# Kernel optimization log

Hardware: AMD Instinct MI355X
Metric: run time of the kernel (lower is better)

The kernel has to match this reference:

```python
import jax, jax.numpy as jnp
import numpy as np

V, E, HS, HD = 32000, 64, 128, 128
S, T = 128, 48


def gru_cell(x, h, Wih, Whh, bih, bhh):
    # torch nn.GRU cell: gates stacked as [r, z, n]
    gi = x @ Wih.T + bih
    gh = h @ Whh.T + bhh
    ir, iz, inn = jnp.split(gi, 3, axis=-1)
    hr, hz, hn = jnp.split(gh, 3, axis=-1)
    r = jax.nn.sigmoid(ir + hr)
    z = jax.nn.sigmoid(iz + hz)
    n = jnp.tanh(inn + r * hn)
    return (1.0 - z) * n + z * h


def setup_inputs() -> dict:
    key = jax.random.key(0)
    ks = jax.random.split(key, 16)
    sc = 0.05
    inp = {
        'document': jax.random.randint(ks[0], (S, T), 0, V, dtype=jnp.int64),
        'enc_emb': jax.random.normal(ks[1], (V, E), jnp.float32) * sc,
        'enc_Wih': jax.random.normal(ks[2], (3 * HS, E), jnp.float32) * sc,
        'enc_Whh': jax.random.normal(ks[3], (3 * HS, HS), jnp.float32) * sc,
        'enc_bih': jax.random.normal(ks[4], (3 * HS,), jnp.float32) * sc,
        'enc_bhh': jax.random.normal(ks[5], (3 * HS,), jnp.float32) * sc,
        'doc_Wih': jax.random.normal(ks[6], (3 * HD, HS), jnp.float32) * sc,
        'doc_Whh': jax.random.normal(ks[7], (3 * HD, HD), jnp.float32) * sc,
        'doc_bih': jax.random.normal(ks[8], (3 * HD,), jnp.float32) * sc,
        'doc_bhh': jax.random.normal(ks[9], (3 * HD,), jnp.float32) * sc,
        'dec_emb': jax.random.normal(ks[10], (V, E), jnp.float32) * sc,
        'dec_Wih': jax.random.normal(ks[11], (3 * HS, E + HD), jnp.float32) * sc,
        'dec_Whh': jax.random.normal(ks[12], (3 * HS, HS), jnp.float32) * sc,
        'dec_bih': jax.random.normal(ks[13], (3 * HS,), jnp.float32) * sc,
        'dec_bhh': jax.random.normal(ks[14], (3 * HS,), jnp.float32) * sc,
        'fc_W': jax.random.normal(ks[15], (V, HS), jnp.float32) * sc,
        'fc_b': jnp.zeros((V,), jnp.float32),
    }
    return inp


def reference(document, enc_emb, enc_Wih, enc_Whh, enc_bih, enc_bhh,
              doc_Wih, doc_Whh, doc_bih, doc_bhh,
              dec_emb, dec_Wih, dec_Whh, dec_bih, dec_bhh, fc_W, fc_b):
    s, t = document.shape
    # --- sentence encoder: GRU over tokens, batch = sentences ---
    x = enc_emb[document]                       # [S, T, E]
    def enc_step(h, xt):
        return gru_cell(xt, h, enc_Wih, enc_Whh, enc_bih, enc_bhh), None
    h0 = jnp.zeros((s, HS), enc_emb.dtype)
    sent_vec, _ = jax.lax.scan(enc_step, h0, jnp.swapaxes(x, 0, 1))  # [S, HS]
    # --- document encoder: GRU over sentence vectors, batch = 1 ---
    def doc_step(h, sv):
        return gru_cell(sv[None, :], h, doc_Wih, doc_Whh, doc_bih, doc_bhh), None
    hd0 = jnp.zeros((1, HD), enc_emb.dtype)
    doc_h, _ = jax.lax.scan(doc_step, hd0, sent_vec)
    doc_vec = doc_h[0]                          # [HD]
    # --- teacher-forced decoder, vectorized over sentences ---
    dec_in = dec_emb[document[:, :-1]]          # [S, T-1, E]
    ctx = jnp.broadcast_to(doc_vec, (s, t - 1, HD))
    xs = jnp.swapaxes(jnp.concatenate([dec_in, ctx], axis=-1), 0, 1)  # [T-1, S, E+HD]
    def dec_step(h, xt):
        h2 = gru_cell(xt, h, dec_Wih, dec_Whh, dec_bih, dec_bhh)
        logits = h2 @ fc_W.T + fc_b
        return h2, logits
    _, logits = jax.lax.scan(dec_step, sent_vec, xs)  # [T-1, S, V]
    targets = document[:, 1:].T                 # [T-1, S]
    logp = jax.nn.log_softmax(logits, axis=-1)
    ll = jnp.take_along_axis(logp, targets[..., None], axis=-1)[..., 0]
    # per-sentence mean over steps, then mean over sentences == global mean
    return -jnp.mean(ll)
```

## Files before the change

kernel.cpp:

```cpp
#include <hip/hip_runtime.h>

typedef unsigned short ushort_t;
typedef short bf16x8 __attribute__((ext_vector_type(8)));
typedef float f32x4 __attribute__((ext_vector_type(4)));
typedef unsigned int u32x4 __attribute__((ext_vector_type(4)));
typedef _Float16 half2t __attribute__((ext_vector_type(2)));

#define LOG2E 1.4426950408889634f
#define LN2   0.6931471805599453f

__device__ __forceinline__ float bf2f(ushort_t u) {
    union { unsigned int i; float f; } v; v.i = ((unsigned int)u) << 16; return v.f;
}
__device__ __forceinline__ ushort_t f2bf(float f) {
    union { float f; unsigned int i; } v; v.f = f;
    unsigned int u = v.i;
    unsigned int r = (u + 0x7FFFu + ((u >> 16) & 1u)) >> 16;
    return (ushort_t)r;
}
__device__ __forceinline__ float hsum4(f32x4 v) { return (v[0] + v[1]) + (v[2] + v[3]); }
__device__ __forceinline__ float frcp(float x) { return __builtin_amdgcn_rcpf(x); }
__device__ __forceinline__ float fsig(float x) { return frcp(1.f + __expf(-x)); }
__device__ __forceinline__ float ftanh(float x) { return 1.f - 2.f * frcp(1.f + __expf(2.f * x)); }
__device__ __forceinline__ int hpad(int e) { return e + ((e >> 4) << 2); }
__device__ __forceinline__ float dot2(unsigned int w, unsigned int h, float acc) {
    union { unsigned int u; half2t h2; } a, b;
    a.u = w; b.u = h;
    return __builtin_amdgcn_fdot2(a.h2, b.h2, acc, false);
}
__device__ __forceinline__ float dpp_xor1_add(float x) {
    int m = __builtin_amdgcn_update_dpp(0, __builtin_bit_cast(int, x), 0xB1, 0xF, 0xF, true);
    return x + __builtin_bit_cast(float, m);
}
__device__ __forceinline__ float dpp_xor2_add(float x) {
    int m = __builtin_amdgcn_update_dpp(0, __builtin_bit_cast(int, x), 0x4E, 0xF, 0xF, true);
    return x + __builtin_bit_cast(float, m);
}
__device__ __forceinline__ ushort_t f2h(float f) {
    union { _Float16 h; ushort_t s; } c; c.h = (_Float16)f; return c.s;
}

__global__ void k_convert(const float* __restrict__ w, ushort_t* __restrict__ o,
                          const float* __restrict__ fcb, float* __restrict__ fcbs) {
    int i = blockIdx.x * blockDim.x + threadIdx.x;
    if (i < 1024000) {
        f32x4 v = ((const f32x4*)w)[i];
        union { ushort_t u[4]; unsigned long long q; } p;
        p.u[0] = f2bf(v[0] * LOG2E); p.u[1] = f2bf(v[1] * LOG2E);
        p.u[2] = f2bf(v[2] * LOG2E); p.u[3] = f2bf(v[3] * LOG2E);
        ((unsigned long long*)o)[i] = p.q;
    } else if (i < 1024000 + 8000) {
        int k = i - 1024000;
        f32x4 b = ((const f32x4*)fcb)[k];
        ((f32x4*)fcbs)[k] = b * LOG2E;
    }
}

__global__ __launch_bounds__(768, 1) void k_encoder(
    const int* __restrict__ doc, const float* __restrict__ emb,
    const float* __restrict__ Wih, const float* __restrict__ Whh,
    const float* __restrict__ bih, const float* __restrict__ bhh,
    float* __restrict__ sent) {
    int s = blockIdx.x, t = threadIdx.x;
    int half = t & 1, j = t >> 1;
    __shared__ float xs[80], hs[160];
    __shared__ float gi[384], gh[384];
    __shared__ int toks[48];
    f32x4 wih[8], whh[16];
#pragma unroll
    for (int k = 0; k < 8; k++) wih[k] = *(const f32x4*)(Wih + j * 64 + half * 32 + k * 4);
#pragma unroll
    for (int k = 0; k < 16; k++) whh[k] = *(const f32x4*)(Whh + j * 128 + half * 64 + k * 4);
    float bi = bih[j], bh = bhh[j];
    if (t < 48) toks[t] = doc[s * 48 + t];
    if (t < 128) hs[hpad(t)] = 0.f;
    __syncthreads();
    if (t < 64) xs[hpad(t)] = emb[(size_t)toks[0] * 64 + t];
    __syncthreads();
    const float* xb = xs + half * 40;
    const float* hb = hs + half * 80;
    for (int tt = 0; tt < 48; tt++) {
        float xnext = (t < 64 && tt + 1 < 48) ? emb[(size_t)toks[tt + 1] * 64 + t] : 0.f;
        f32x4 a0 = {0,0,0,0}, b0 = {0,0,0,0}, b1 = {0,0,0,0};
#pragma unroll
        for (int k = 0; k < 8; k++) a0 += wih[k] * (*(const f32x4*)(xb + k * 4 + (k >> 2) * 4));
#pragma unroll
        for (int k = 0; k < 16; k += 2) {
            b0 += whh[k] * (*(const f32x4*)(hb + k * 4 + (k >> 2) * 4));
            b1 += whh[k + 1] * (*(const f32x4*)(hb + (k + 1) * 4 + ((k + 1) >> 2) * 4));
        }
        float a = hsum4(a0), b = hsum4(b0 + b1);
        a = dpp_xor1_add(a); b = dpp_xor1_add(b);
        if (half == 0) { gi[j] = a + bi; gh[j] = b + bh; }
        __syncthreads();
        if (t < 128) {
            float r = fsig(gi[t] + gh[t]);
            float z = fsig(gi[t + 128] + gh[t + 128]);
            float n = ftanh(gi[t + 256] + r * gh[t + 256]);
            hs[hpad(t)] = (1.f - z) * n + z * hs[hpad(t)];
        }
        if (t < 64 && tt + 1 < 48) xs[hpad(t)] = xnext;
        __syncthreads();
    }
    if (t < 128) sent[s * 128 + t] = hs[hpad(t)];
}

__global__ void k_doc_gi(const float* __restrict__ sv, const float* __restrict__ Wih,
                         const float* __restrict__ bih, float* __restrict__ gidoc,
                         const float* __restrict__ Whh, ushort_t* __restrict__ wdoc) {
    int bid = blockIdx.x, j = threadIdx.x;
    if (bid >= 128) {
        int i = (bid - 128) * 384 + j;
        if (i < 12288) {
            f32x4 v = ((const f32x4*)Whh)[i];
            union { ushort_t u[4]; unsigned long long q; } p;
            p.u[0] = f2h(v[0]); p.u[1] = f2h(v[1]); p.u[2] = f2h(v[2]); p.u[3] = f2h(v[3]);
            ((unsigned long long*)wdoc)[i] = p.q;
        }
        return;
    }
    __shared__ f32x4 v4[32];
    if (j < 128) ((float*)v4)[j] = sv[bid * 128 + j];
    __syncthreads();
    f32x4 a0 = {0,0,0,0}, a1 = {0,0,0,0};
#pragma unroll
    for (int k = 0; k < 32; k += 2) {
        a0 += *(const f32x4*)(Wih + j * 128 + k * 4) * v4[k];
        a1 += *(const f32x4*)(Wih + j * 128 + (k + 1) * 4) * v4[k + 1];
    }
    gidoc[bid * 384 + j] = bih[j] + hsum4(a0 + a1);
}

__global__ __launch_bounds__(512, 1) __attribute__((amdgpu_waves_per_eu(1, 2)))
void k_doc_seq(
    const float* __restrict__ gidoc, const ushort_t* __restrict__ wdoc,
    const float* __restrict__ bhh, float* __restrict__ dvec) {
    int t = threadIdx.x, q = t & 3, e = t >> 2;
    __shared__ unsigned int hpk[2][64];
    u32x4 wr4[4], wz4[4], wn4[4];
    const ushort_t* wbase = wdoc + e * 128 + q * 32;
#pragma unroll
    for (int k = 0; k < 4; k++) {
        wr4[k] = *(const u32x4*)(wbase + k * 8);
        wz4[k] = *(const u32x4*)(wbase + 128 * 128 + k * 8);
        wn4[k] = *(const u32x4*)(wbase + 256 * 128 + k * 8);
    }
    float biasr = bhh[e], biasz = bhh[128 + e], biasn = bhh[256 + e];
    float cr = gidoc[e], cz = gidoc[128 + e], cn = gidoc[256 + e];
    if (t < 64) hpk[0][t] = 0u;
    float he = 0.f;
    __syncthreads();
    for (int i = 0; i < 128; i++) {
        float nr = 0.f, nz = 0.f, nn = 0.f;
        if (i + 1 < 128) {
            const float* g = gidoc + (i + 1) * 384;
            nr = g[e]; nz = g[128 + e]; nn = g[256 + e];
        }
        const unsigned int* hp = &hpk[i & 1][q * 16];
        u32x4 hv[4];
        hv[0] = *(const u32x4*)(hp);
        hv[1] = *(const u32x4*)(hp + 4);
        hv[2] = *(const u32x4*)(hp + 8);
        hv[3] = *(const u32x4*)(hp + 12);
        float ra0 = 0.f, ra1 = 0.f, za0 = 0.f, za1 = 0.f, na0 = 0.f, na1 = 0.f;
#pragma unroll
        for (int k = 0; k < 4; k++) {
            u32x4 h4 = hv[k];
            ra0 = dot2(wr4[k][0], h4[0], ra0); ra1 = dot2(wr4[k][1], h4[1], ra1);
            ra0 = dot2(wr4[k][2], h4[2], ra0); ra1 = dot2(wr4[k][3], h4[3], ra1);
            za0 = dot2(wz4[k][0], h4[0], za0); za1 = dot2(wz4[k][1], h4[1], za1);
            za0 = dot2(wz4[k][2], h4[2], za0); za1 = dot2(wz4[k][3], h4[3], za1);
            na0 = dot2(wn4[k][0], h4[0], na0); na1 = dot2(wn4[k][1], h4[1], na1);
            na0 = dot2(wn4[k][2], h4[2], na0); na1 = dot2(wn4[k][3], h4[3], na1);
        }
        float rp = ra0 + ra1, zp = za0 + za1, np = na0 + na1;
        rp = dpp_xor2_add(dpp_xor1_add(rp));
        zp = dpp_xor2_add(dpp_xor1_add(zp));
        np = dpp_xor2_add(dpp_xor1_add(np));
        float r = fsig(cr + rp + biasr);
        float z = fsig(cz + zp + biasz);
        float n = ftanh(cn + r * (np + biasn));
        he = (1.f - z) * n + z * he;
        if (q == 0) ((ushort_t*)&hpk[(i & 1) ^ 1][0])[e] = f2h(he);
        __syncthreads();
        cr = nr; cz = nz; cn = nn;
    }
    if (q == 0) dvec[e] = he;
}

__global__ __launch_bounds__(768, 1) void k_dec_gi(
    const int* __restrict__ doc, const float* __restrict__ emb,
    const float* __restrict__ Wih, const float* __restrict__ bih,
    const float* __restrict__ dvec, float* __restrict__ gidec) {
    int s = blockIdx.x, t = threadIdx.x, half = t & 1, j = t >> 1;
    __shared__ float xs[80], dvs[160];
    __shared__ int toks[48];
    f32x4 wih[8];
#pragma unroll
    for (int k = 0; k < 8; k++) wih[k] = *(const f32x4*)(Wih + j * 192 + half * 32 + k * 4);
    if (t < 128) dvs[hpad(t)] = dvec[t];
    if (t < 47) toks[t] = doc[s * 48 + t];
    __syncthreads();
    f32x4 c0 = {0,0,0,0}, c1 = {0,0,0,0};
    const float* dp = dvs + half * 80;
#pragma unroll
    for (int k = 0; k < 16; k += 2) {
        c0 += (*(const f32x4*)(Wih + j * 192 + 64 + half * 64 + k * 4)) *
              (*(const f32x4*)(dp + k * 4 + (k >> 2) * 4));
        c1 += (*(const f32x4*)(Wih + j * 192 + 64 + half * 64 + (k + 1) * 4)) *
              (*(const f32x4*)(dp + (k + 1) * 4 + ((k + 1) >> 2) * 4));
    }
    float g = hsum4(c0 + c1);
    g = dpp_xor1_add(g);
    g += bih[j];
    if (t < 64) xs[hpad(t)] = emb[(size_t)toks[0] * 64 + t];
    __syncthreads();
    const float* xb = xs + half * 40;
    for (int tt = 0; tt < 47; tt++) {
        float xnext = (t < 64 && tt + 1 < 47) ? emb[(size_t)toks[tt + 1] * 64 + t] : 0.f;
        f32x4 a0 = {0,0,0,0};
#pragma unroll
        for (int k = 0; k < 8; k++) a0 += wih[k] * (*(const f32x4*)(xb + k * 4 + (k >> 2) * 4));
        float a = hsum4(a0);
        a = dpp_xor1_add(a);
        if (half == 0) gidec[(tt * 128 + s) * 384 + j] = g + a;
        __syncthreads();
        if (t < 64 && tt + 1 < 47) xs[hpad(t)] = xnext;
        __syncthreads();
    }
}

__global__ __launch_bounds__(768, 1) void k_dec_seq(
    const float* __restrict__ gidec, const float* __restrict__ Whh,
    const float* __restrict__ bhh, const float* __restrict__ sent,
    ushort_t* __restrict__ h2b) {
    int s = blockIdx.x, t = threadIdx.x, half = t & 1, j = t >> 1;
    __shared__ float hs[160];
    __shared__ float gi[384], gh[384];
    f32x4 whh[16];
#pragma unroll
    for (int k = 0; k < 16; k++) whh[k] = *(const f32x4*)(Whh + j * 128 + half * 64 + k * 4);
    float bh = bhh[j];
    if (t < 128) hs[hpad(t)] = sent[s * 128 + t];
    float gval = (half == 0) ? gidec[s * 384 + j] : 0.f;
    __syncthreads();
    const float* hb = hs + half * 80;
    for (int i = 0; i < 47; i++) {
        float gnext = (half == 0 && i + 1 < 47) ? gidec[((i + 1) * 128 + s) * 384 + j] : 0.f;
        f32x4 b0 = {0,0,0,0}, b1 = {0,0,0,0};
#pragma unroll
        for (int k = 0; k < 16; k += 2) {
            b0 += whh[k] * (*(const f32x4*)(hb + k * 4 + (k >> 2) * 4));
            b1 += whh[k + 1] * (*(const f32x4*)(hb + (k + 1) * 4 + ((k + 1) >> 2) * 4));
        }
        float b = hsum4(b0 + b1);
        b = dpp_xor1_add(b);
        if (half == 0) { gh[j] = b + bh; gi[j] = gval; }
        __syncthreads();
        if (t < 128) {
            float r = fsig(gi[t] + gh[t]);
            float z = fsig(gi[t + 128] + gh[t + 128]);
            float n = ftanh(gi[t + 256] + r * gh[t + 256]);
            float hn = (1.f - z) * n + z * hs[hpad(t)];
            hs[hpad(t)] = hn;
            h2b[(i * 128 + s) * 128 + t] = f2bf(hn);
        }
        __syncthreads();
        gval = gnext;
    }
}

__global__ void k_tl(const int* __restrict__ doc, const ushort_t* __restrict__ h2b,
                     const ushort_t* __restrict__ wb, const float* __restrict__ fcb,
                     float* __restrict__ tl) {
    int r = blockIdx.x * 4 + (threadIdx.x >> 6);
    int lane = threadIdx.x & 63;
    int s = r & 127, t = r >> 7;
    int tok = doc[s * 48 + t + 1];
    const ushort_t* hp = h2b + r * 128;
    const ushort_t* wp = wb + tok * 128;
    float acc = bf2f(hp[lane]) * bf2f(wp[lane]) + bf2f(hp[lane + 64]) * bf2f(wp[lane + 64]);
#pragma unroll
    for (int m = 32; m >= 1; m >>= 1) acc += __shfl_xor(acc, m);
    if (lane == 0) tl[r] = acc * LN2 + fcb[tok];
}

#define LSE_VC 10
#define LSE_NC 3200
#define LSE_NPAIR 25
__global__ __launch_bounds__(512, 2) void k_lse(
    const ushort_t* __restrict__ h2b, const ushort_t* __restrict__ wb,
    const float* __restrict__ fcbs, float* __restrict__ parts) {
    int rb = blockIdx.x / LSE_VC;
    int vc = blockIdx.x % LSE_VC;
    int t = threadIdx.x;
    int wave = t >> 6, lane = t & 63;
    int rg = wave >> 1, cg = wave & 1;
    int q = lane >> 4, l15 = lane & 15;

    __shared__ __align__(16) char ldsB[65536];

    int row0 = rb * 128 + rg * 32;
    bf16x8 a[2][4];
    const ushort_t* ap = h2b + (size_t)(row0 + l15) * 128 + q * 8;
#pragma unroll
    for (int m = 0; m < 2; m++)
#pragma unroll
        for (int c = 0; c < 4; c++) a[m][c] = *(const bf16x8*)(ap + m * 2048 + c * 32);

    const char* wbB = (const char*)wb;
    int so = ((t >> 4) << 8) + (((t & 15) ^ ((t >> 4) & 15)) << 4);
    char* dst1 = ldsB + wave * 1024;

#define LSE_STAGE(buf, cb) do { \
    const char* g_ = wbB + (size_t)(cb) * 256 + so; \
    char* d_ = dst1 + (buf) * 16384; \
    __builtin_amdgcn_global_load_lds((const __attribute__((address_space(1))) unsigned int*)(g_), \
                                     (__attribute__((address_space(3))) unsigned int*)(d_), 16, 0, 0); \
    __builtin_amdgcn_global_load_lds((const __attribute__((address_space(1))) unsigned int*)(g_ + 8192), \
                                     (__attribute__((address_space(3))) unsigned int*)(d_ + 8192), 16, 0, 0); \
} while (0)

    int ra[2][4];
#pragma unroll
    for (int c2 = 0; c2 < 2; c2++)
#pragma unroll
        for (int c = 0; c < 4; c++)
            ra[c2][c] = (cg * 32 + c2 * 16 + l15) * 256 + (((q + 4 * c) ^ l15) << 4);

    int cb0 = vc * LSE_NC;
    f32x4 se[2] = {{0,0,0,0},{0,0,0,0}};

    LSE_STAGE(0, cb0);
    LSE_STAGE(1, cb0 + 64);
    __syncthreads();
    int cur = 0;
    for (int it = 0; it < LSE_NPAIR; ++it) {
        if (it + 1 < LSE_NPAIR) {
            LSE_STAGE(2 * (cur ^ 1),     cb0 + (2 * it + 2) * 64);
            LSE_STAGE(2 * (cur ^ 1) + 1, cb0 + (2 * it + 3) * 64);
        }
        int colg = cb0 + 2 * it * 64 + cg * 32 + l15;
        float bA0 = fcbs[colg],      bA1 = fcbs[colg + 16];
        float bB0 = fcbs[colg + 64], bB1 = fcbs[colg + 80];
#pragma unroll
        for (int half = 0; half < 2; half++) {
            const char* bb = ldsB + (size_t)(2 * cur + half) * 16384;
            float bs0 = half ? bB0 : bA0;
            float bs1 = half ? bB1 : bA1;
            f32x4 acc[2][2] = {{{0,0,0,0},{0,0,0,0}},{{0,0,0,0},{0,0,0,0}}};
#pragma unroll
            for (int c = 0; c < 4; c++) {
                bf16x8 b0 = *(const bf16x8*)(bb + ra[0][c]);
                bf16x8 b1 = *(const bf16x8*)(bb + ra[1][c]);
                acc[0][0] = __builtin_amdgcn_mfma_f32_16x16x32_bf16(a[0][c], b0, acc[0][0], 0, 0, 0);
                acc[1][0] = __builtin_amdgcn_mfma_f32_16x16x32_bf16(a[1][c], b0, acc[1][0], 0, 0, 0);
                acc[0][1] = __builtin_amdgcn_mfma_f32_16x16x32_bf16(a[0][c], b1, acc[0][1], 0, 0, 0);
                acc[1][1] = __builtin_amdgcn_mfma_f32_16x16x32_bf16(a[1][c], b1, acc[1][1], 0, 0, 0);
            }
#pragma unroll
            for (int m = 0; m < 2; m++) {
#pragma unroll
                for (int r = 0; r < 4; r++)
                    se[m][r] += __builtin_amdgcn_exp2f(acc[m][0][r] + bs0)
                              + __builtin_amdgcn_exp2f(acc[m][1][r] + bs1);
            }
        }
        __syncthreads();
        cur ^= 1;
    }

#pragma unroll
    for (int m = 0; m < 2; m++) {
        f32x4 v = se[m];
#pragma unroll
        for (int d = 1; d < 16; d <<= 1) {
            v[0] += __shfl_xor(v[0], d);
            v[1] += __shfl_xor(v[1], d);
            v[2] += __shfl_xor(v[2], d);
            v[3] += __shfl_xor(v[3], d);
        }
        if (l15 == 0) {
            float* p = parts + (size_t)(vc * 2 + cg) * 6016 + row0 + m * 16 + q * 4;
            p[0] = v[0]; p[1] = v[1]; p[2] = v[2]; p[3] = v[3];
        }
    }
}

__global__ void k_final1(const float* __restrict__ parts, const float* __restrict__ tl,
                         float* __restrict__ rowloss) {
    int r = blockIdx.x * 128 + threadIdx.x;
    float tot = 0.f;
#pragma unroll 4
    for (int c = 0; c < 20; c++) tot += parts[(size_t)c * 6016 + r];
    rowloss[r] = logf(tot) - tl[r];
}

__global__ void k_final2(const float* __restrict__ rowloss, float* __restrict__ out) {
    __shared__ float red[512];
    int tid = threadIdx.x;
    float acc = 0.f;
    for (int r = tid; r < 6016; r += 512) acc += rowloss[r];
    red[tid] = acc;
    __syncthreads();
    for (int s = 256; s > 0; s >>= 1) {
        if (tid < s) red[tid] += red[tid + s];
        __syncthreads();
    }
    if (tid == 0) out[0] = red[0] / 6016.f;
}

extern "C" void kernel_launch(void* const* d_in, const int* in_sizes, int n_in,
                              void* d_out, int out_size, void* d_ws, size_t ws_size,
                              hipStream_t stream) {
    const int* doc = (const int*)d_in[0];
    const float* enc_emb = (const float*)d_in[1];
    const float* enc_Wih = (const float*)d_in[2];
    const float* enc_Whh = (const float*)d_in[3];
    const float* enc_bih = (const float*)d_in[4];
    const float* enc_bhh = (const float*)d_in[5];
    const float* doc_Wih = (const float*)d_in[6];
    const float* doc_Whh = (const float*)d_in[7];
    const float* doc_bih = (const float*)d_in[8];
    const float* doc_bhh = (const float*)d_in[9];
    const float* dec_emb = (const float*)d_in[10];
    const float* dec_Wih = (const float*)d_in[11];
    const float* dec_Whh = (const float*)d_in[12];
    const float* dec_bih = (const float*)d_in[13];
    const float* dec_bhh = (const float*)d_in[14];
    const float* fc_W = (const float*)d_in[15];
    const float* fc_b = (const float*)d_in[16];

    char* ws = (char*)d_ws;
    ushort_t* fcWb = (ushort_t*)(ws + 0);
    float* sent    = (float*)(ws + 8192000);
    float* dvec    = (float*)(ws + 8257536);
    float* gidoc   = (float*)(ws + 8258048);
    float* gidec   = (float*)(ws + 8456192);
    ushort_t* h2b  = (ushort_t*)(ws + 17696768);
    float* tl      = (float*)(ws + 19236864);
    float* parts   = (float*)(ws + 19260928);
    float* rowloss = (float*)(ws + 20223488);
    ushort_t* wdoc = (ushort_t*)(ws + 20247552);
    float* fcbs    = (float*)(ws + 20345856);
    float* out = (float*)d_out;

    k_convert<<<4032, 256, 0, stream>>>(fc_W, fcWb, fc_b, fcbs);
    k_encoder<<<128, 768, 0, stream>>>(doc, enc_emb, enc_Wih, enc_Whh, enc_bih, enc_bhh, sent);
    k_doc_gi<<<160, 384, 0, stream>>>(sent, doc_Wih, doc_bih, gidoc, doc_Whh, wdoc);
    k_doc_seq<<<1, 512, 0, stream>>>(gidoc, wdoc, doc_bhh, dvec);
    k_dec_gi<<<128, 768, 0, stream>>>(doc, dec_emb, dec_Wih, dec_bih, dvec, gidec);
    k_dec_seq<<<128, 768, 0, stream>>>(gidec, dec_Whh, dec_bhh, sent, h2b);
    k_tl<<<1504, 256, 0, stream>>>(doc, h2b, fcWb, fc_b, tl);
    k_lse<<<47 * LSE_VC, 512, 0, stream>>>(h2b, fcWb, fcbs, parts);
    k_final1<<<47, 128, 0, stream>>>(parts, tl, rowloss);
    k_final2<<<1, 512, 0, stream>>>(rowloss, out);
}
```

Measured before the change: 267.5 us.

## Merge doc GRU, decoder input projection and fc_W conversion into one launch

Combines the serial single-block document GRU, the decoder embedding-input projection and the fc_W bf16 conversion into one kernel with role-split blocks. The independent stages can then run concurrently instead of one after another behind the long serial doc recurrence. To make the decoder input projection independent of the document vector, the context term (dec_Wih context columns times doc_vec, plus bias) moves to a tiny new kernel and is added in the decoder sequence kernel. The cost is one extra small launch and a mixed-role kernel whose block scheduling order decides how much overlap is actually achieved.

```diff
diff --git a/kernel.cpp b/kernel.cpp
--- a/kernel.cpp
+++ b/kernel.cpp
@@ -38,22 +38,6 @@
 }
 __device__ __forceinline__ ushort_t f2h(float f) {
     union { _Float16 h; ushort_t s; } c; c.h = (_Float16)f; return c.s;
-}
-
-__global__ void k_convert(const float* __restrict__ w, ushort_t* __restrict__ o,
-                          const float* __restrict__ fcb, float* __restrict__ fcbs) {
-    int i = blockIdx.x * blockDim.x + threadIdx.x;
-    if (i < 1024000) {
-        f32x4 v = ((const f32x4*)w)[i];
-        union { ushort_t u[4]; unsigned long long q; } p;
-        p.u[0] = f2bf(v[0] * LOG2E); p.u[1] = f2bf(v[1] * LOG2E);
-        p.u[2] = f2bf(v[2] * LOG2E); p.u[3] = f2bf(v[3] * LOG2E);
-        ((unsigned long long*)o)[i] = p.q;
-    } else if (i < 1024000 + 8000) {
-        int k = i - 1024000;
-        f32x4 b = ((const f32x4*)fcb)[k];
-        ((f32x4*)fcbs)[k] = b * LOG2E;
-    }
 }
 
 __global__ __launch_bounds__(768, 1) void k_encoder(
@@ -132,108 +116,134 @@
 }
 
 __global__ __launch_bounds__(512, 1) __attribute__((amdgpu_waves_per_eu(1, 2)))
-void k_doc_seq(
+void k_mid(
     const float* __restrict__ gidoc, const ushort_t* __restrict__ wdoc,
-    const float* __restrict__ bhh, float* __restrict__ dvec) {
-    int t = threadIdx.x, q = t & 3, e = t >> 2;
-    __shared__ unsigned int hpk[2][64];
-    u32x4 wr4[4], wz4[4], wn4[4];
-    const ushort_t* wbase = wdoc + e * 128 + q * 32;
-#pragma unroll
-    for (int k = 0; k < 4; k++) {
-        wr4[k] = *(const u32x4*)(wbase + k * 8);
-        wz4[k] = *(const u32x4*)(wbase + 128 * 128 + k * 8);
-        wn4[k] = *(const u32x4*)(wbase + 256 * 128 + k * 8);
-    }
-    float biasr = bhh[e], biasz = bhh[128 + e], biasn = bhh[256 + e];
-    float cr = gidoc[e], cz = gidoc[128 + e], cn = gidoc[256 + e];
-    if (t < 64) hpk[0][t] = 0u;
-    float he = 0.f;
-    __syncthreads();
-    for (int i = 0; i < 128; i++) {
-        float nr = 0.f, nz = 0.f, nn = 0.f;
-        if (i + 1 < 128) {
-            const float* g = gidoc + (i + 1) * 384;
-            nr = g[e]; nz = g[128 + e]; nn = g[256 + e];
-        }
-        const unsigned int* hp = &hpk[i & 1][q * 16];
-        u32x4 hv[4];
-        hv[0] = *(const u32x4*)(hp);
-        hv[1] = *(const u32x4*)(hp + 4);
-        hv[2] = *(const u32x4*)(hp + 8);
-        hv[3] = *(const u32x4*)(hp + 12);
-        float ra0 = 0.f, ra1 = 0.f, za0 = 0.f, za1 = 0.f, na0 = 0.f, na1 = 0.f;
+    const float* __restrict__ dbhh, float* __restrict__ dvec,
+    const int* __restrict__ doc, const float* __restrict__ demb,
+    const float* __restrict__ dWih, float* __restrict__ gidec,
+    const float* __restrict__ fcW, ushort_t* __restrict__ fcWb,
+    const float* __restrict__ fcb, float* __restrict__ fcbs) {
+    int bid = blockIdx.x, t = threadIdx.x;
+
+    if (bid == 0) {
+        int q = t & 3, e = t >> 2;
+        __shared__ unsigned int hpk[2][64];
+        u32x4 wr4[4], wz4[4], wn4[4];
+        const ushort_t* wbase = wdoc + e * 128 + q * 32;
 #pragma unroll
         for (int k = 0; k < 4; k++) {
-            u32x4 h4 = hv[k];
-            ra0 = dot2(wr4[k][0], h4[0], ra0); ra1 = dot2(wr4[k][1], h4[1], ra1);
-            ra0 = dot2(wr4[k][2], h4[2], ra0); ra1 = dot2(wr4[k][3], h4[3], ra1);
-            za0 = dot2(wz4[k][0], h4[0], za0); za1 = dot2(wz4[k][1], h4[1], za1);
-            za0 = dot2(wz4[k][2], h4[2], za0); za1 = dot2(wz4[k][3], h4[3], za1);
-            na0 = dot2(wn4[k][0], h4[0], na0); na1 = dot2(wn4[k][1], h4[1], na1);
-            na0 = dot2(wn4[k][2], h4[2], na0); na1 = dot2(wn4[k][3], h4[3], na1);
-        }
-        float rp = ra0 + ra1, zp = za0 + za1, np = na0 + na1;
-        rp = dpp_xor2_add(dpp_xor1_add(rp));
-        zp = dpp_xor2_add(dpp_xor1_add(zp));
-        np = dpp_xor2_add(dpp_xor1_add(np));
-        float r = fsig(cr + rp + biasr);
-        float z = fsig(cz + zp + biasz);
-        float n = ftanh(cn + r * (np + biasn));
-        he = (1.f - z) * n + z * he;
-        if (q == 0) ((ushort_t*)&hpk[(i & 1) ^ 1][0])[e] = f2h(he);
-        __syncthreads();
-        cr = nr; cz = nz; cn = nn;
-    }
-    if (q == 0) dvec[e] = he;
-}
-
-__global__ __launch_bounds__(768, 1) void k_dec_gi(
-    const int* __restrict__ doc, const float* __restrict__ emb,
-    const float* __restrict__ Wih, const float* __restrict__ bih,
-    const float* __restrict__ dvec, float* __restrict__ gidec) {
-    int s = blockIdx.x, t = threadIdx.x, half = t & 1, j = t >> 1;
-    __shared__ float xs[80], dvs[160];
-    __shared__ int toks[48];
-    f32x4 wih[8];
-#pragma unroll
-    for (int k = 0; k < 8; k++) wih[k] = *(const f32x4*)(Wih + j * 192 + half * 32 + k * 4);
-    if (t < 128) dvs[hpad(t)] = dvec[t];
-    if (t < 47) toks[t] = doc[s * 48 + t];
-    __syncthreads();
-    f32x4 c0 = {0,0,0,0}, c1 = {0,0,0,0};
-    const float* dp = dvs + half * 80;
-#pragma unroll
-    for (int k = 0; k < 16; k += 2) {
-        c0 += (*(const f32x4*)(Wih + j * 192 + 64 + half * 64 + k * 4)) *
-              (*(const f32x4*)(dp + k * 4 + (k >> 2) * 4));
-        c1 += (*(const f32x4*)(Wih + j * 192 + 64 + half * 64 + (k + 1) * 4)) *
-              (*(const f32x4*)(dp + (k + 1) * 4 + ((k + 1) >> 2) * 4));
-    }
-    float g = hsum4(c0 + c1);
-    g = dpp_xor1_add(g);
-    g += bih[j];
-    if (t < 64) xs[hpad(t)] = emb[(size_t)toks[0] * 64 + t];
-    __syncthreads();
-    const float* xb = xs + half * 40;
-    for (int tt = 0; tt < 47; tt++) {
-        float xnext = (t < 64 && tt + 1 < 47) ? emb[(size_t)toks[tt + 1] * 64 + t] : 0.f;
-        f32x4 a0 = {0,0,0,0};
-#pragma unroll
-        for (int k = 0; k < 8; k++) a0 += wih[k] * (*(const f32x4*)(xb + k * 4 + (k >> 2) * 4));
-        float a = hsum4(a0);
-        a = dpp_xor1_add(a);
-        if (half == 0) gidec[(tt * 128 + s) * 384 + j] = g + a;
-        __syncthreads();
-        if (t < 64 && tt + 1 < 47) xs[hpad(t)] = xnext;
-        __syncthreads();
-    }
+            wr4[k] = *(const u32x4*)(wbase + k * 8);
+            wz4[k] = *(const u32x4*)(wbase + 128 * 128 + k * 8);
+            wn4[k] = *(const u32x4*)(wbase + 256 * 128 + k * 8);
+        }
+        float biasr = dbhh[e], biasz = dbhh[128 + e], biasn = dbhh[256 + e];
+        float cr = gidoc[e], cz = gidoc[128 + e], cn = gidoc[256 + e];
+        if (t < 64) hpk[0][t] = 0u;
+        float he = 0.f;
+        __syncthreads();
+        for (int i = 0; i < 128; i++) {
+            float nr = 0.f, nz = 0.f, nn = 0.f;
+            if (i + 1 < 128) {
+                const float* g = gidoc + (i + 1) * 384;
+                nr = g[e]; nz = g[128 + e]; nn = g[256 + e];
+            }
+            const unsigned int* hp = &hpk[i & 1][q * 16];
+            u32x4 hv[4];
+            hv[0] = *(const u32x4*)(hp);
+            hv[1] = *(const u32x4*)(hp + 4);
+            hv[2] = *(const u32x4*)(hp + 8);
+            hv[3] = *(const u32x4*)(hp + 12);
+            float ra0 = 0.f, ra1 = 0.f, za0 = 0.f, za1 = 0.f, na0 = 0.f, na1 = 0.f;
+#pragma unroll
+            for (int k = 0; k < 4; k++) {
+                u32x4 h4 = hv[k];
+                ra0 = dot2(wr4[k][0], h4[0], ra0); ra1 = dot2(wr4[k][1], h4[1], ra1);
+                ra0 = dot2(wr4[k][2], h4[2], ra0); ra1 = dot2(wr4[k][3], h4[3], ra1);
+                za0 = dot2(wz4[k][0], h4[0], za0); za1 = dot2(wz4[k][1], h4[1], za1);
+                za0 = dot2(wz4[k][2], h4[2], za0); za1 = dot2(wz4[k][3], h4[3], za1);
+                na0 = dot2(wn4[k][0], h4[0], na0); na1 = dot2(wn4[k][1], h4[1], na1);
+                na0 = dot2(wn4[k][2], h4[2], na0); na1 = dot2(wn4[k][3], h4[3], na1);
+            }
+            float rp = ra0 + ra1, zp = za0 + za1, np = na0 + na1;
+            rp = dpp_xor2_add(dpp_xor1_add(rp));
+            zp = dpp_xor2_add(dpp_xor1_add(zp));
+            np = dpp_xor2_add(dpp_xor1_add(np));
+            float r = fsig(cr + rp + biasr);
+            float z = fsig(cz + zp + biasz);
+            float n = ftanh(cn + r * (np + biasn));
+            he = (1.f - z) * n + z * he;
+            if (q == 0) ((ushort_t*)&hpk[(i & 1) ^ 1][0])[e] = f2h(he);
+            __syncthreads();
+            cr = nr; cz = nz; cn = nn;
+        }
+        if (q == 0) dvec[e] = he;
+        return;
+    }
+
+    if (bid <= 128) {
+        int s = bid - 1;
+        __shared__ float xs[80];
+        __shared__ int toks[48];
+        if (t < 47) toks[t] = doc[s * 48 + t];
+        __syncthreads();
+        if (t < 64) xs[hpad(t)] = demb[(size_t)toks[0] * 64 + t];
+        __syncthreads();
+        f32x4 wih[16];
+        if (t < 384) {
+#pragma unroll
+            for (int k = 0; k < 16; k++) wih[k] = *(const f32x4*)(dWih + t * 192 + k * 4);
+        }
+        for (int tt = 0; tt < 47; tt++) {
+            float xnext = (t < 64 && tt + 1 < 47) ? demb[(size_t)toks[tt + 1] * 64 + t] : 0.f;
+            if (t < 384) {
+                f32x4 a0 = {0,0,0,0}, a1 = {0,0,0,0};
+#pragma unroll
+                for (int k = 0; k < 16; k += 2) {
+                    a0 += wih[k] * (*(const f32x4*)(xs + k * 4 + (k >> 2) * 4));
+                    a1 += wih[k + 1] * (*(const f32x4*)(xs + (k + 1) * 4 + ((k + 1) >> 2) * 4));
+                }
+                gidec[(tt * 128 + s) * 384 + t] = hsum4(a0 + a1);
+            }
+            __syncthreads();
+            if (t < 64 && tt + 1 < 47) xs[hpad(t)] = xnext;
+            __syncthreads();
+        }
+        return;
+    }
+
+    int i = (bid - 129) * 512 + t;
+    if (i < 1024000) {
+        f32x4 v = ((const f32x4*)fcW)[i];
+        union { ushort_t u[4]; unsigned long long qq; } p;
+        p.u[0] = f2bf(v[0] * LOG2E); p.u[1] = f2bf(v[1] * LOG2E);
+        p.u[2] = f2bf(v[2] * LOG2E); p.u[3] = f2bf(v[3] * LOG2E);
+        ((unsigned long long*)fcWb)[i] = p.qq;
+    } else if (i < 1024000 + 8000) {
+        int k = i - 1024000;
+        f32x4 b = ((const f32x4*)fcb)[k];
+        ((f32x4*)fcbs)[k] = b * LOG2E;
+    }
+}
+
+__global__ void k_gctx(const float* __restrict__ Wih, const float* __restrict__ bih,
+                       const float* __restrict__ dvec, float* __restrict__ gctx) {
+    int j = threadIdx.x;
+    __shared__ f32x4 v4[32];
+    if (j < 128) ((float*)v4)[j] = dvec[j];
+    __syncthreads();
+    f32x4 a0 = {0,0,0,0}, a1 = {0,0,0,0};
+#pragma unroll
+    for (int k = 0; k < 32; k += 2) {
+        a0 += *(const f32x4*)(Wih + j * 192 + 64 + k * 4) * v4[k];
+        a1 += *(const f32x4*)(Wih + j * 192 + 64 + (k + 1) * 4) * v4[k + 1];
+    }
+    gctx[j] = bih[j] + hsum4(a0 + a1);
 }
 
 __global__ __launch_bounds__(768, 1) void k_dec_seq(
     const float* __restrict__ gidec, const float* __restrict__ Whh,
     const float* __restrict__ bhh, const float* __restrict__ sent,
-    ushort_t* __restrict__ h2b) {
+    const float* __restrict__ gctx, ushort_t* __restrict__ h2b) {
     int s = blockIdx.x, t = threadIdx.x, half = t & 1, j = t >> 1;
     __shared__ float hs[160];
     __shared__ float gi[384], gh[384];
@@ -241,12 +251,13 @@
 #pragma unroll
     for (int k = 0; k < 16; k++) whh[k] = *(const f32x4*)(Whh + j * 128 + half * 64 + k * 4);
     float bh = bhh[j];
+    float g_me = gctx[j];
     if (t < 128) hs[hpad(t)] = sent[s * 128 + t];
-    float gval = (half == 0) ? gidec[s * 384 + j] : 0.f;
+    float gval = (half == 0) ? (gidec[s * 384 + j] + g_me) : 0.f;
     __syncthreads();
     const float* hb = hs + half * 80;
     for (int i = 0; i < 47; i++) {
-        float gnext = (half == 0 && i + 1 < 47) ? gidec[((i + 1) * 128 + s) * 384 + j] : 0.f;
+        float gnext = (half == 0 && i + 1 < 47) ? (gidec[((i + 1) * 128 + s) * 384 + j] + g_me) : 0.f;
         f32x4 b0 = {0,0,0,0}, b1 = {0,0,0,0};
 #pragma unroll
         for (int k = 0; k < 16; k += 2) {
@@ -443,14 +454,16 @@
     float* rowloss = (float*)(ws + 20223488);
     ushort_t* wdoc = (ushort_t*)(ws + 20247552);
     float* fcbs    = (float*)(ws + 20345856);
+    float* gctx    = (float*)(ws + 20473856);
     float* out = (float*)d_out;
 
-    k_convert<<<4032, 256, 0, stream>>>(fc_W, fcWb, fc_b, fcbs);
     k_encoder<<<128, 768, 0, stream>>>(doc, enc_emb, enc_Wih, enc_Whh, enc_bih, enc_bhh, sent);
     k_doc_gi<<<160, 384, 0, stream>>>(sent, doc_Wih, doc_bih, gidoc, doc_Whh, wdoc);
-    k_doc_seq<<<1, 512, 0, stream>>>(gidoc, wdoc, doc_bhh, dvec);
-    k_dec_gi<<<128, 768, 0, stream>>>(doc, dec_emb, dec_Wih, dec_bih, dvec, gidec);
-    k_dec_seq<<<128, 768, 0, stream>>>(gidec, dec_Whh, dec_bhh, sent, h2b);
+    k_mid<<<1 + 128 + 2016, 512, 0, stream>>>(gidoc, wdoc, doc_bhh, dvec,
+                                              doc, dec_emb, dec_Wih, gidec,
+                                              fc_W, fcWb, fc_b, fcbs);
+    k_gctx<<<1, 384, 0, stream>>>(dec_Wih, dec_bih, dvec, gctx);
+    k_dec_seq<<<128, 768, 0, stream>>>(gidec, dec_Whh, dec_bhh, sent, gctx, h2b);
     k_tl<<<1504, 256, 0, stream>>>(doc, h2b, fcWb, fc_b, tl);
     k_lse<<<47 * LSE_VC, 512, 0, stream>>>(h2b, fcWb, fcbs, parts);
     k_final1<<<47, 128, 0, stream>>>(parts, tl, rowloss);
```

New measurement: 252.4 us. 1.06x faster.
